# Optimization experiments

Measured on AMD Instinct MI355X. Metric: run time of the kernel, lower is better.

## Reference

```python
import jax, jax.numpy as jnp
import numpy as np

B, T, D, H = 4, 1024, 512, 8
DK = D // H
L = 2 * T - 1  # relative-position length, Transformer-XL convention


def setup_inputs() -> dict:
    key = jax.random.key(0)
    ks = jax.random.split(key, 16)
    s = 0.02  # xavier-ish init scale
    inp = {
        "query": jax.random.normal(ks[0], (B, T, D), jnp.float32),
        "key": jax.random.normal(ks[1], (B, T, D), jnp.float32),
        "value": jax.random.normal(ks[2], (B, T, D), jnp.float32),
        "pos_embedding": jax.random.normal(ks[3], (B, L, D), jnp.float32),
        "mask": jax.random.randint(ks[4], (B, T), 0, 2).astype(bool),
        # nn.Linear weights are [out, in]; y = x @ W.T + b
        "Wq": jax.random.normal(ks[5], (D, D), jnp.float32) * s,
        "bq": jnp.zeros((D,), jnp.float32),
        "Wk": jax.random.normal(ks[6], (D, D), jnp.float32) * s,
        "bk": jnp.zeros((D,), jnp.float32),
        "Wv": jax.random.normal(ks[7], (D, D), jnp.float32) * s,
        "bv": jnp.zeros((D,), jnp.float32),
        "Wr": jax.random.normal(ks[8], (D, D), jnp.float32) * s,  # rpe_proj, no bias
        "u_bias": jax.random.normal(ks[9], (H, DK), jnp.float32) * s,
        "v_bias": jax.random.normal(ks[10], (H, DK), jnp.float32) * s,
        "Wo": jax.random.normal(ks[11], (D, D), jnp.float32) * s,
        "bo": jnp.zeros((D,), jnp.float32),
    }
    return inp


def _rel_shift(x):
    # x: [B, H, T, L] -> Transformer-XL pad/reshape/slice shift, keep first L//2+1 cols
    b, h, t, l = x.shape
    x = jnp.pad(x, ((0, 0), (0, 0), (0, 0), (1, 0)))        # [B,H,T,L+1]
    x = x.reshape(b, h, l + 1, t)[:, :, 1:, :]               # drop first row
    x = x.reshape(b, h, t, l)
    return x[..., : l // 2 + 1]                              # [B,H,T,T]


def reference(query, key, value, pos_embedding, mask,
              Wq, bq, Wk, bk, Wv, bv, Wr, u_bias, v_bias, Wo, bo):
    b = query.shape[0]
    q = (query @ Wq.T + bq).reshape(b, -1, H, DK)            # [B,T,H,dk]
    k = (key @ Wk.T + bk).reshape(b, -1, H, DK)              # [B,T,H,dk]
    v = (value @ Wv.T + bv).reshape(b, -1, H, DK)            # [B,T,H,dk]
    r = (pos_embedding @ Wr.T).reshape(b, -1, H, DK)         # [B,L,H,dk]

    main = jnp.einsum('bthd,bshd->bhts', q + u_bias, k)      # content score
    rpe = jnp.einsum('bthd,blhd->bhtl', q + v_bias, r)       # [B,H,T,L]

    scores = (main + _rel_shift(rpe)) / np.sqrt(DK).astype(np.float32)
    scores = jnp.where(mask[:, None, None, :],
                       jnp.asarray(1e-4, scores.dtype), scores)
    attn = jax.nn.softmax(scores, axis=-1)                   # dropout off (eval)

    out = jnp.einsum('bhts,bshd->bhtd', attn, v)             # [B,H,T,dk]
    # Faithful to original: view(B,-1,d_model) WITHOUT transposing heads back
    out = out.reshape(b, -1, D)                              # [B,T,D] (head-interleaved)
    return out @ Wo.T + bo
```

## Files before the change

### kernel.cpp

```cpp
#include <hip/hip_runtime.h>
#include <stdint.h>
#include <stddef.h>

#define B_ 4
#define T_ 1024
#define D_ 512
#define H_ 8
#define DK_ 64
#define L_ 2047
#define LP_ 2048

typedef __attribute__((ext_vector_type(8))) short short8;
typedef __attribute__((ext_vector_type(4))) short short4_t;
typedef __attribute__((ext_vector_type(4))) float f32x4;
typedef __attribute__((ext_vector_type(8))) __bf16 bf16x8;

static __device__ __forceinline__ short f2bf(float f) {
  union { float f; unsigned u; } x; x.f = f;
  unsigned r = x.u + 0x7fffu + ((x.u >> 16) & 1u);
  return (short)(r >> 16);
}

static __device__ __forceinline__ f32x4 mfma16(bf16x8 a, bf16x8 b, f32x4 c) {
  return __builtin_amdgcn_mfma_f32_16x16x32_bf16(a, b, c, 0, 0, 0);
}

static __device__ __forceinline__ bf16x8 ldbf8(const short* p) {
  return *(const bf16x8*)p;
}

__global__ __launch_bounds__(256) void convert_kernel(
    const float* __restrict__ qin, const float* __restrict__ kin, const float* __restrict__ vin,
    const float* __restrict__ pin,
    const float* __restrict__ Wq, const float* __restrict__ Wk, const float* __restrict__ Wv,
    const float* __restrict__ Wr, const float* __restrict__ Wo,
    const unsigned char* __restrict__ mraw,
    short* __restrict__ dst, float* __restrict__ mask_f)
{
  if (blockIdx.x == 11518) {
    __shared__ int fmis, fany;
    if (threadIdx.x == 0) { fmis = 0; fany = 0; }
    __syncthreads();
    int lm = 0, la = 0;
    for (int i = threadIdx.x; i < B_ * T_; i += 256) {
      unsigned char c = mraw[i];
      if (c) { la = 1; if (i & 3) lm = 1; }
    }
    if (lm) atomicOr(&fmis, 1);
    if (la) atomicOr(&fany, 1);
    __syncthreads();
    int mmode = fmis ? 0 : (fany ? 1 : 2);
    const int* mi = (const int*)mraw;
    for (int i = threadIdx.x; i < B_ * T_; i += 256) {
      int mv = (mmode == 0) ? (int)mraw[i] : (mmode == 1 ? mi[i] : 0);
      mask_f[i] = mv ? 1.0f : 0.0f;
    }
    return;
  }
  int gid = blockIdx.x * 256 + threadIdx.x;
  const float* src; int base;
  if      (gid < 524288)  { src = qin; base = 0; }
  else if (gid < 1048576) { src = kin; base = 524288; }
  else if (gid < 1572864) { src = vin; base = 1048576; }
  else if (gid < 2620928) { src = pin; base = 1572864; }
  else if (gid < 2686464) { src = Wq;  base = 2620928; }
  else if (gid < 2752000) { src = Wk;  base = 2686464; }
  else if (gid < 2817536) { src = Wv;  base = 2752000; }
  else if (gid < 2883072) { src = Wr;  base = 2817536; }
  else                    { src = Wo;  base = 2883072; }
  f32x4 val = ((const f32x4*)src)[gid - base];
  short4_t o;
  o[0] = f2bf(val[0]); o[1] = f2bf(val[1]); o[2] = f2bf(val[2]); o[3] = f2bf(val[3]);
  ((short4_t*)dst)[gid] = o;
}

__global__ __launch_bounds__(256) void proj_gemm(
    const short* __restrict__ qkv_bf, const short* __restrict__ pos_bf,
    const short* __restrict__ W_bf, const short* __restrict__ ao_bf,
    int variant,
    short* __restrict__ quO, short* __restrict__ qvO, short* __restrict__ khO,
    short* __restrict__ vtO, short* __restrict__ rhO, float* __restrict__ outF,
    const float* __restrict__ bq, const float* __restrict__ bk_,
    const float* __restrict__ bv_, const float* __restrict__ bo_,
    const float* __restrict__ ub, const float* __restrict__ vb)
{
  const int bid = blockIdx.x;
  const short* A; const short* W;
  int Mtotal, mode, m0, n0;
  if (variant == 0) {
    if (bid < 768) {
      int zz = bid >> 8, r2 = bid & 255;
      m0 = (r2 >> 3) * 128; n0 = (r2 & 7) * 64;
      A = qkv_bf + (size_t)zz * 2097152; W = W_bf + (size_t)zz * 262144;
      Mtotal = 4096; mode = zz;
    } else {
      int r2 = bid - 768;
      m0 = (r2 >> 3) * 128; n0 = (r2 & 7) * 64;
      A = pos_bf; W = W_bf + 786432;
      Mtotal = 8188; mode = 3;
    }
  } else {
    m0 = (bid >> 3) * 128; n0 = (bid & 7) * 64;
    A = ao_bf; W = W_bf + 1048576;
    Mtotal = 4096; mode = 4;
  }
  __shared__ __align__(16) short As[2][128 * 64];
  __shared__ __align__(16) short Bs[2][64 * 64];
  const int tid = threadIdx.x;
  const int lane = tid & 63, wid = tid >> 6;
  const int wr = wid >> 1, wc = wid & 1;
  const int l15 = lane & 15, l4 = lane >> 4;

  const int trow = tid >> 3;
  const int tcol = (((tid & 7) ^ (trow & 7)) << 3);
  const int wbase = wid * 512;

  auto STAGE = [&](int buf, int kt) {
#pragma unroll
    for (int j = 0; j < 4; j++) {
      int row = j * 32 + trow;
      int srow = m0 + row; if (srow > Mtotal - 1) srow = Mtotal - 1;
      __builtin_amdgcn_global_load_lds(
          (const __attribute__((address_space(1))) unsigned int*)(A + (size_t)srow * 512 + kt + tcol),
          (__attribute__((address_space(3))) unsigned int*)(&As[buf][j * 2048 + wbase]), 16, 0, 0);
    }
#pragma unroll
    for (int j = 0; j < 2; j++) {
      int row = j * 32 + trow;
      __builtin_amdgcn_global_load_lds(
          (const __attribute__((address_space(1))) unsigned int*)(W + (size_t)(n0 + row) * 512 + kt + tcol),
          (__attribute__((address_space(3))) unsigned int*)(&Bs[buf][j * 2048 + wbase]), 16, 0, 0);
    }
  };

  f32x4 acc[4][2] = {};
  STAGE(0, 0);
  __syncthreads();

  for (int it = 0; it < 8; ++it) {
    const int cur = it & 1;
    if (it < 7) STAGE(cur ^ 1, (it + 1) * 64);
    __builtin_amdgcn_s_setprio(1);
#pragma unroll
    for (int kf = 0; kf < 2; kf++) {
      const int colA = ((kf * 4 + l4) ^ (l15 & 7)) << 3;
      bf16x8 af[4], bf2[2];
#pragma unroll
      for (int rf = 0; rf < 4; rf++)
        af[rf] = ldbf8(&As[cur][(wr * 64 + rf * 16 + l15) * 64 + colA]);
#pragma unroll
      for (int cf = 0; cf < 2; cf++)
        bf2[cf] = ldbf8(&Bs[cur][(wc * 32 + cf * 16 + l15) * 64 + colA]);
#pragma unroll
      for (int rf = 0; rf < 4; rf++)
#pragma unroll
        for (int cf = 0; cf < 2; cf++)
          acc[rf][cf] = mfma16(af[rf], bf2[cf], acc[rf][cf]);
    }
    __builtin_amdgcn_s_setprio(0);
    __syncthreads();
  }

#pragma unroll
  for (int cf = 0; cf < 2; cf++) {
    int n = n0 + wc * 32 + cf * 16 + l15;
    float bias = 0.f, ubv = 0.f, vbv = 0.f;
    if (mode == 0) { bias = bq[n]; ubv = ub[n]; vbv = vb[n]; }
    else if (mode == 1) bias = bk_[n];
    else if (mode == 2) bias = bv_[n];
    else if (mode == 4) bias = bo_[n];
    int hh = n >> 6, dk = n & 63;
#pragma unroll
    for (int rf = 0; rf < 4; rf++) {
#pragma unroll
      for (int reg = 0; reg < 4; reg++) {
        int m = m0 + wr * 64 + rf * 16 + l4 * 4 + reg;
        float val = acc[rf][cf][reg] + bias;
        if (mode == 0) {
          int bb = m >> 10, t = m & 1023;
          size_t ad = ((size_t)(bb * H_ + hh) * T_ + t) * DK_ + dk;
          quO[ad] = f2bf(val + ubv);
          qvO[ad] = f2bf(val + vbv);
        } else if (mode == 1) {
          int bb = m >> 10, t = m & 1023;
          khO[((size_t)(bb * H_ + hh) * T_ + t) * DK_ + dk] = f2bf(val);
        } else if (mode == 2) {
          int bb = m >> 10, t = m & 1023;
          vtO[((size_t)(bb * H_ + hh) * DK_ + dk) * T_ + t] = f2bf(val);
        } else if (mode == 3) {
          if (m < B_ * L_) {
            int bb = m / L_;
            int ll = m - bb * L_;
            rhO[((size_t)(bb * H_ + hh) * LP_ + ll) * DK_ + dk] = f2bf(val);
          }
        } else {
          outF[(size_t)m * D_ + n] = val;
        }
      }
    }
  }
}

__global__ __launch_bounds__(256) void attn_kernel(
    const short* __restrict__ qu, const short* __restrict__ qv,
    const short* __restrict__ kh, const short* __restrict__ vt,
    const short* __restrict__ rh, const float* __restrict__ mask_f,
    short* __restrict__ attnout)
{
  const int tid = threadIdx.x;
  const int lane = tid & 63;
  const int w = tid >> 6;
  const int l15 = lane & 15, l4 = lane >> 4;
  const int bid = blockIdx.x;
  const int xcd = bid & 7, slot = bid >> 3;
  const int bh = (slot >> 4) * 8 + xcd;
  const int b = bh >> 3;
  const int t0b = (slot & 15) * 64;
  const int t0w = t0b + w * 16;
  const int woff = 48 - w * 16;

  __shared__ __align__(16) short Ks[2][64 * 64];
  __shared__ __align__(16) short Vs[2][64 * 64];
  __shared__ __align__(16) short Rs[2][128 * 64];
  __shared__ __align__(16) short Ps[4][16 * 64];

  const short* kB = kh + (size_t)bh * T_ * DK_;
  const short* vB = vt + (size_t)bh * DK_ * T_;
  const short* rB = rh + (size_t)bh * LP_ * DK_;
  const float* mB = mask_f + b * T_;

  const short* quB = qu + ((size_t)bh * T_ + t0w + l15) * DK_ + l4 * 8;
  const short* qvB = qv + ((size_t)bh * T_ + t0w + l15) * DK_ + l4 * 8;
  bf16x8 quf0 = ldbf8(quB), quf1 = ldbf8(quB + 32);
  bf16x8 qvf0 = ldbf8(qvB), qvf1 = ldbf8(qvB + 32);

  const short8 ones_s = {(short)0x3F80, (short)0x3F80, (short)0x3F80, (short)0x3F80,
                         (short)0x3F80, (short)0x3F80, (short)0x3F80, (short)0x3F80};
  const bf16x8 ones8 = __builtin_bit_cast(bf16x8, ones_s);

  const int trow = tid >> 3;
  const int tcol = (((tid & 7) ^ ((tid >> 3) & 7)) << 3);
  const int wbase = w * 512;

  auto STAGE = [&](int buf, int s0) {
    const int l0b = 960 + s0 - t0b;
#pragma unroll
    for (int j = 0; j < 2; j++) {
      __builtin_amdgcn_global_load_lds(
          (const __attribute__((address_space(1))) unsigned int*)(kB + (size_t)(s0 + trow + j * 32) * 64 + tcol),
          (__attribute__((address_space(3))) unsigned int*)(&Ks[buf][j * 2048 + wbase]), 16, 0, 0);
      __builtin_amdgcn_global_load_lds(
          (const __attribute__((address_space(1))) unsigned int*)(vB + (size_t)(trow + j * 32) * T_ + s0 + tcol),
          (__attribute__((address_space(3))) unsigned int*)(&Vs[buf][j * 2048 + wbase]), 16, 0, 0);
    }
#pragma unroll
    for (int j = 0; j < 4; j++) {
      __builtin_amdgcn_global_load_lds(
          (const __attribute__((address_space(1))) unsigned int*)(rB + (size_t)(l0b + trow + j * 32) * 64 + tcol),
          (__attribute__((address_space(3))) unsigned int*)(&Rs[buf][j * 2048 + wbase]), 16, 0, 0);
    }
  };

  f32x4 accO[4] = {};
  f32x4 sum_acc = {};

  STAGE(0, 0);
  __syncthreads();

  const int swz = (l15 & 7) << 3;

  for (int it = 0; it < 16; ++it) {
    const int s0 = it << 6;
    const int cur = it & 1;
    if (it < 15) STAGE(cur ^ 1, s0 + 64);

    float mk[4];
#pragma unroll
    for (int cf = 0; cf < 4; cf++) mk[cf] = mB[s0 + cf * 16 + l15];

    f32x4 sacc[4] = {};
    f32x4 gacc[5] = {};
    __builtin_amdgcn_s_setprio(1);
#pragma unroll
    for (int kf = 0; kf < 2; kf++) {
      const int col = (kf * 32 + l4 * 8) ^ swz;
      bf16x8 qf = kf ? quf1 : quf0;
      bf16x8 vf_ = kf ? qvf1 : qvf0;
#pragma unroll
      for (int cf = 0; cf < 4; cf++)
        sacc[cf] = mfma16(qf, ldbf8(&Ks[cur][(cf * 16 + l15) * 64 + col]), sacc[cf]);
#pragma unroll
      for (int gf = 0; gf < 5; gf++)
        gacc[gf] = mfma16(vf_, ldbf8(&Rs[cur][(woff + gf * 16 + l15) * 64 + col]), gacc[gf]);
    }
    __builtin_amdgcn_s_setprio(0);

    float p[4][4];
#pragma unroll
    for (int r = 0; r < 4; r++) {
      const int tl = l4 * 4 + r;
      const int e = l15 + 15 - tl;
      const int src = (lane & 48) | (e & 15);
      float sh0 = __shfl(gacc[0][r], src);
      float sh1 = __shfl(gacc[1][r], src);
      float sh2 = __shfl(gacc[2][r], src);
      float sh3 = __shfl(gacc[3][r], src);
      float sh4 = __shfl(gacc[4][r], src);
      float ga[4] = {sh0, sh1, sh2, sh3};
      float gb[4] = {sh1, sh2, sh3, sh4};
#pragma unroll
      for (int cf = 0; cf < 4; cf++) {
        float gg = (e < 16) ? ga[cf] : gb[cf];
        float lg = (sacc[cf][r] + gg) * 0.125f;
        lg = (mk[cf] != 0.f) ? 1e-4f : lg;
        p[r][cf] = __expf(lg);
      }
    }

#pragma unroll
    for (int r = 0; r < 4; r++) {
      const int tl = l4 * 4 + r;
      const int sw2 = (tl & 7) << 3;
#pragma unroll
      for (int cf = 0; cf < 4; cf++)
        Ps[w][tl * 64 + ((cf * 16 + l15) ^ sw2)] = f2bf(p[r][cf]);
    }

    __builtin_amdgcn_s_setprio(1);
#pragma unroll
    for (int kf = 0; kf < 2; kf++) {
      const int kc = kf * 32 + l4 * 8;
      bf16x8 pa = ldbf8(&Ps[w][l15 * 64 + (kc ^ swz)]);
      sum_acc = mfma16(pa, ones8, sum_acc);
#pragma unroll
      for (int vf = 0; vf < 4; vf++)
        accO[vf] = mfma16(pa, ldbf8(&Vs[cur][(vf * 16 + l15) * 64 + (kc ^ swz)]), accO[vf]);
    }
    __builtin_amdgcn_s_setprio(0);
    __syncthreads();
  }

#pragma unroll
  for (int r = 0; r < 4; r++) {
    const int tl = l4 * 4 + r;
    float inv = 1.0f / sum_acc[r];
#pragma unroll
    for (int vf = 0; vf < 4; vf++) {
      float val = accO[vf][r] * inv;
      attnout[((size_t)bh * T_ + t0w + tl) * DK_ + vf * 16 + l15] = f2bf(val);
    }
  }
}

extern "C" void kernel_launch(void* const* d_in, const int* in_sizes, int n_in,
                              void* d_out, int out_size, void* d_ws, size_t ws_size,
                              hipStream_t stream) {
  const float* qin = (const float*)d_in[0];
  const float* kin = (const float*)d_in[1];
  const float* vin = (const float*)d_in[2];
  const float* pin = (const float*)d_in[3];
  const unsigned char* mraw = (const unsigned char*)d_in[4];
  const float* Wq = (const float*)d_in[5];
  const float* bq = (const float*)d_in[6];
  const float* Wk = (const float*)d_in[7];
  const float* bk = (const float*)d_in[8];
  const float* Wv = (const float*)d_in[9];
  const float* bv = (const float*)d_in[10];
  const float* Wr = (const float*)d_in[11];
  const float* ub = (const float*)d_in[12];
  const float* vb = (const float*)d_in[13];
  const float* Wo = (const float*)d_in[14];
  const float* bo = (const float*)d_in[15];
  float* out = (float*)d_out;
  char* ws = (char*)d_ws;

  short* qkv_bf = (short*)(ws + 0);
  short* pos_bf = (short*)(ws + 12582912);
  short* W_bf   = (short*)(ws + 20967424);
  float* mask_f = (float*)(ws + 23588864);
  short* quW    = (short*)(ws + 23605248);
  short* qvW    = (short*)(ws + 27799552);
  short* khW    = (short*)(ws + 31993856);
  short* vtW    = (short*)(ws + 36188160);
  short* rhW    = (short*)(ws + 40382464);
  short* aoW    = (short*)(ws + 48771072);

  convert_kernel<<<dim3(11519), dim3(256), 0, stream>>>(
      qin, kin, vin, pin, Wq, Wk, Wv, Wr, Wo, mraw, qkv_bf, mask_f);
  proj_gemm<<<dim3(1280), dim3(256), 0, stream>>>(
      qkv_bf, pos_bf, W_bf, aoW, 0, quW, qvW, khW, vtW, rhW, nullptr,
      bq, bk, bv, bo, ub, vb);
  attn_kernel<<<dim3(512), dim3(256), 0, stream>>>(
      quW, qvW, khW, vtW, rhW, mask_f, aoW);
  proj_gemm<<<dim3(256), dim3(256), 0, stream>>>(
      qkv_bf, pos_bf, W_bf, aoW, 1, quW, qvW, khW, vtW, rhW, out,
      bq, bk, bv, bo, ub, vb);
}
```

Baseline: 109.8 us.

## Fuse fp32-to-bf16 activation conversion into projection GEMM A-tile staging

The separate conversion pass over query/key/value/pos_embedding is removed. The projection GEMM now loads fp32 A tiles into registers, converts them with packed bf16 conversion instructions, and writes them to swizzled LDS after the MFMA loop, so the prefetch overlaps compute. This drops a large bf16 write and re-read of activations. The weight-only convert kernel stays, the GEMM is templated on variant, and block indices are remapped so consecutive blocks land on different XCD-strided tiles. The cost is doubled global A-read bytes in the GEMM (fp32 instead of bf16), plus extra register pressure and a VALU conversion step.

```diff
diff --git a/kernel.cpp b/kernel.cpp
--- a/kernel.cpp
+++ b/kernel.cpp
@@ -13,6 +13,7 @@
 typedef __attribute__((ext_vector_type(8))) short short8;
 typedef __attribute__((ext_vector_type(4))) short short4_t;
 typedef __attribute__((ext_vector_type(4))) float f32x4;
+typedef __attribute__((ext_vector_type(4))) unsigned int u32x4;
 typedef __attribute__((ext_vector_type(8))) __bf16 bf16x8;
 
 static __device__ __forceinline__ short f2bf(float f) {
@@ -21,6 +22,12 @@
   return (short)(r >> 16);
 }
 
+static __device__ __forceinline__ unsigned cvtpk(float lo, float hi) {
+  unsigned r;
+  asm("v_cvt_pk_bf16_f32 %0, %1, %2" : "=v"(r) : "v"(lo), "v"(hi));
+  return r;
+}
+
 static __device__ __forceinline__ f32x4 mfma16(bf16x8 a, bf16x8 b, f32x4 c) {
   return __builtin_amdgcn_mfma_f32_16x16x32_bf16(a, b, c, 0, 0, 0);
 }
@@ -29,15 +36,13 @@
   return *(const bf16x8*)p;
 }
 
-__global__ __launch_bounds__(256) void convert_kernel(
-    const float* __restrict__ qin, const float* __restrict__ kin, const float* __restrict__ vin,
-    const float* __restrict__ pin,
+__global__ __launch_bounds__(256) void convertW_kernel(
     const float* __restrict__ Wq, const float* __restrict__ Wk, const float* __restrict__ Wv,
     const float* __restrict__ Wr, const float* __restrict__ Wo,
     const unsigned char* __restrict__ mraw,
-    short* __restrict__ dst, float* __restrict__ mask_f)
+    short* __restrict__ W_bf, float* __restrict__ mask_f)
 {
-  if (blockIdx.x == 11518) {
+  if (blockIdx.x == 1280) {
     __shared__ int fmis, fany;
     if (threadIdx.x == 0) { fmis = 0; fany = 0; }
     __syncthreads();
@@ -59,49 +64,50 @@
   }
   int gid = blockIdx.x * 256 + threadIdx.x;
   const float* src; int base;
-  if      (gid < 524288)  { src = qin; base = 0; }
-  else if (gid < 1048576) { src = kin; base = 524288; }
-  else if (gid < 1572864) { src = vin; base = 1048576; }
-  else if (gid < 2620928) { src = pin; base = 1572864; }
-  else if (gid < 2686464) { src = Wq;  base = 2620928; }
-  else if (gid < 2752000) { src = Wk;  base = 2686464; }
-  else if (gid < 2817536) { src = Wv;  base = 2752000; }
-  else if (gid < 2883072) { src = Wr;  base = 2817536; }
-  else                    { src = Wo;  base = 2883072; }
+  if      (gid <  65536) { src = Wq; base = 0; }
+  else if (gid < 131072) { src = Wk; base = 65536; }
+  else if (gid < 196608) { src = Wv; base = 131072; }
+  else if (gid < 262144) { src = Wr; base = 196608; }
+  else                   { src = Wo; base = 262144; }
   f32x4 val = ((const f32x4*)src)[gid - base];
   short4_t o;
   o[0] = f2bf(val[0]); o[1] = f2bf(val[1]); o[2] = f2bf(val[2]); o[3] = f2bf(val[3]);
-  ((short4_t*)dst)[gid] = o;
-}
-
+  ((short4_t*)W_bf)[gid] = o;
+}
+
+template<int VARIANT>
 __global__ __launch_bounds__(256) void proj_gemm(
-    const short* __restrict__ qkv_bf, const short* __restrict__ pos_bf,
+    const float* __restrict__ qin, const float* __restrict__ kin,
+    const float* __restrict__ vin, const float* __restrict__ pin,
     const short* __restrict__ W_bf, const short* __restrict__ ao_bf,
-    int variant,
     short* __restrict__ quO, short* __restrict__ qvO, short* __restrict__ khO,
     short* __restrict__ vtO, short* __restrict__ rhO, float* __restrict__ outF,
     const float* __restrict__ bq, const float* __restrict__ bk_,
     const float* __restrict__ bv_, const float* __restrict__ bo_,
     const float* __restrict__ ub, const float* __restrict__ vb)
 {
-  const int bid = blockIdx.x;
-  const short* A; const short* W;
+  const int bid0 = blockIdx.x;
+  constexpr int PER = (VARIANT == 0) ? 160 : 32;
+  const int bid = (bid0 & 7) * PER + (bid0 >> 3);
+
+  const float* Afp = nullptr; const short* Abf = nullptr; const short* W;
   int Mtotal, mode, m0, n0;
-  if (variant == 0) {
+  if constexpr (VARIANT == 0) {
     if (bid < 768) {
       int zz = bid >> 8, r2 = bid & 255;
       m0 = (r2 >> 3) * 128; n0 = (r2 & 7) * 64;
-      A = qkv_bf + (size_t)zz * 2097152; W = W_bf + (size_t)zz * 262144;
+      Afp = (zz == 0) ? qin : (zz == 1) ? kin : vin;
+      W = W_bf + (size_t)zz * 262144;
       Mtotal = 4096; mode = zz;
     } else {
       int r2 = bid - 768;
       m0 = (r2 >> 3) * 128; n0 = (r2 & 7) * 64;
-      A = pos_bf; W = W_bf + 786432;
+      Afp = pin; W = W_bf + 786432;
       Mtotal = 8188; mode = 3;
     }
   } else {
     m0 = (bid >> 3) * 128; n0 = (bid & 7) * 64;
-    A = ao_bf; W = W_bf + 1048576;
+    Abf = ao_bf; W = W_bf + 1048576;
     Mtotal = 4096; mode = 4;
   }
   __shared__ __align__(16) short As[2][128 * 64];
@@ -110,36 +116,61 @@
   const int lane = tid & 63, wid = tid >> 6;
   const int wr = wid >> 1, wc = wid & 1;
   const int l15 = lane & 15, l4 = lane >> 4;
-
   const int trow = tid >> 3;
-  const int tcol = (((tid & 7) ^ (trow & 7)) << 3);
+  const int s8 = tid & 7;
+  const int tcolsw = ((s8 ^ (trow & 7)) << 3);
   const int wbase = wid * 512;
 
-  auto STAGE = [&](int buf, int kt) {
+  f32x4 va[4][2];
+  auto LOADA = [&](int kt) {
 #pragma unroll
     for (int j = 0; j < 4; j++) {
-      int row = j * 32 + trow;
-      int srow = m0 + row; if (srow > Mtotal - 1) srow = Mtotal - 1;
+      int srow = m0 + j * 32 + trow; if (srow > Mtotal - 1) srow = Mtotal - 1;
+      const f32x4* p = (const f32x4*)(Afp + (size_t)srow * 512 + kt + s8 * 8);
+      va[j][0] = p[0]; va[j][1] = p[1];
+    }
+  };
+  auto WRITEA = [&](int buf) {
+#pragma unroll
+    for (int j = 0; j < 4; j++) {
+      u32x4 wv;
+      wv[0] = cvtpk(va[j][0][0], va[j][0][1]);
+      wv[1] = cvtpk(va[j][0][2], va[j][0][3]);
+      wv[2] = cvtpk(va[j][1][0], va[j][1][1]);
+      wv[3] = cvtpk(va[j][1][2], va[j][1][3]);
+      *(u32x4*)&As[buf][(j * 32 + trow) * 64 + tcolsw] = wv;
+    }
+  };
+  auto STAGEA1 = [&](int buf, int kt) {
+#pragma unroll
+    for (int j = 0; j < 4; j++) {
+      int srow = m0 + j * 32 + trow; if (srow > 4095) srow = 4095;
       __builtin_amdgcn_global_load_lds(
-          (const __attribute__((address_space(1))) unsigned int*)(A + (size_t)srow * 512 + kt + tcol),
+          (const __attribute__((address_space(1))) unsigned int*)(Abf + (size_t)srow * 512 + kt + tcolsw),
           (__attribute__((address_space(3))) unsigned int*)(&As[buf][j * 2048 + wbase]), 16, 0, 0);
     }
+  };
+  auto STAGEW = [&](int buf, int kt) {
 #pragma unroll
     for (int j = 0; j < 2; j++) {
       int row = j * 32 + trow;
       __builtin_amdgcn_global_load_lds(
-          (const __attribute__((address_space(1))) unsigned int*)(W + (size_t)(n0 + row) * 512 + kt + tcol),
+          (const __attribute__((address_space(1))) unsigned int*)(W + (size_t)(n0 + row) * 512 + kt + tcolsw),
           (__attribute__((address_space(3))) unsigned int*)(&Bs[buf][j * 2048 + wbase]), 16, 0, 0);
     }
   };
 
   f32x4 acc[4][2] = {};
-  STAGE(0, 0);
+  if constexpr (VARIANT == 0) { LOADA(0); STAGEW(0, 0); WRITEA(0); }
+  else                        { STAGEA1(0, 0); STAGEW(0, 0); }
   __syncthreads();
 
   for (int it = 0; it < 8; ++it) {
     const int cur = it & 1;
-    if (it < 7) STAGE(cur ^ 1, (it + 1) * 64);
+    if (it < 7) {
+      if constexpr (VARIANT == 0) { LOADA((it + 1) * 64); STAGEW(cur ^ 1, (it + 1) * 64); }
+      else                        { STAGEA1(cur ^ 1, (it + 1) * 64); STAGEW(cur ^ 1, (it + 1) * 64); }
+    }
     __builtin_amdgcn_s_setprio(1);
 #pragma unroll
     for (int kf = 0; kf < 2; kf++) {
@@ -158,6 +189,7 @@
           acc[rf][cf] = mfma16(af[rf], bf2[cf], acc[rf][cf]);
     }
     __builtin_amdgcn_s_setprio(0);
+    if constexpr (VARIANT == 0) { if (it < 7) WRITEA(cur ^ 1); }
     __syncthreads();
   }
 
@@ -374,8 +406,6 @@
   float* out = (float*)d_out;
   char* ws = (char*)d_ws;
 
-  short* qkv_bf = (short*)(ws + 0);
-  short* pos_bf = (short*)(ws + 12582912);
   short* W_bf   = (short*)(ws + 20967424);
   float* mask_f = (float*)(ws + 23588864);
   short* quW    = (short*)(ws + 23605248);
@@ -385,14 +415,14 @@
   short* rhW    = (short*)(ws + 40382464);
   short* aoW    = (short*)(ws + 48771072);
 
-  convert_kernel<<<dim3(11519), dim3(256), 0, stream>>>(
-      qin, kin, vin, pin, Wq, Wk, Wv, Wr, Wo, mraw, qkv_bf, mask_f);
-  proj_gemm<<<dim3(1280), dim3(256), 0, stream>>>(
-      qkv_bf, pos_bf, W_bf, aoW, 0, quW, qvW, khW, vtW, rhW, nullptr,
+  convertW_kernel<<<dim3(1281), dim3(256), 0, stream>>>(
+      Wq, Wk, Wv, Wr, Wo, mraw, W_bf, mask_f);
+  proj_gemm<0><<<dim3(1280), dim3(256), 0, stream>>>(
+      qin, kin, vin, pin, W_bf, aoW, quW, qvW, khW, vtW, rhW, nullptr,
       bq, bk, bv, bo, ub, vb);
   attn_kernel<<<dim3(512), dim3(256), 0, stream>>>(
       quW, qvW, khW, vtW, rhW, mask_f, aoW);
-  proj_gemm<<<dim3(256), dim3(256), 0, stream>>>(
-      qkv_bf, pos_bf, W_bf, aoW, 1, quW, qvW, khW, vtW, rhW, out,
+  proj_gemm<1><<<dim3(256), dim3(256), 0, stream>>>(
+      qin, kin, vin, pin, W_bf, aoW, quW, qvW, khW, vtW, rhW, out,
       bq, bk, bv, bo, ub, vb);
 }
```

Result: faster. 97.12 us (-11.5%).

## Triple-buffer projection GEMM with vmcnt waits and XCD-aware block remap

Applied to the files above, without the earlier changes.

The projection GEMM moves from a two-stage to a three-stage LDS ring. Each iteration waits on a partial vmcnt count and one barrier, replacing the full __syncthreads after every step, so two tiles stay in flight during compute. Block IDs are remapped so that blocks with consecutive blockIdx values, which go to different XCDs, work on tiles that are far apart, and each XCD gets a contiguous run of tiles that share A and W data in its L2. The variant argument becomes a template parameter, and the extra buffer raises LDS per block from 48KB to 72KB, which may lower occupancy.

```diff
diff --git a/kernel.cpp b/kernel.cpp
--- a/kernel.cpp
+++ b/kernel.cpp
@@ -13,6 +13,7 @@
 typedef __attribute__((ext_vector_type(8))) short short8;
 typedef __attribute__((ext_vector_type(4))) short short4_t;
 typedef __attribute__((ext_vector_type(4))) float f32x4;
+typedef __attribute__((ext_vector_type(4))) unsigned int u32x4;
 typedef __attribute__((ext_vector_type(8))) __bf16 bf16x8;
 
 static __device__ __forceinline__ short f2bf(float f) {
@@ -74,20 +75,23 @@
   ((short4_t*)dst)[gid] = o;
 }
 
+template<int VARIANT>
 __global__ __launch_bounds__(256) void proj_gemm(
     const short* __restrict__ qkv_bf, const short* __restrict__ pos_bf,
     const short* __restrict__ W_bf, const short* __restrict__ ao_bf,
-    int variant,
     short* __restrict__ quO, short* __restrict__ qvO, short* __restrict__ khO,
     short* __restrict__ vtO, short* __restrict__ rhO, float* __restrict__ outF,
     const float* __restrict__ bq, const float* __restrict__ bk_,
     const float* __restrict__ bv_, const float* __restrict__ bo_,
     const float* __restrict__ ub, const float* __restrict__ vb)
 {
-  const int bid = blockIdx.x;
+  const int bid0 = blockIdx.x;
+  constexpr int PER = (VARIANT == 0) ? 160 : 32;
+  const int bid = (bid0 & 7) * PER + (bid0 >> 3);
+
   const short* A; const short* W;
   int Mtotal, mode, m0, n0;
-  if (variant == 0) {
+  if constexpr (VARIANT == 0) {
     if (bid < 768) {
       int zz = bid >> 8, r2 = bid & 255;
       m0 = (r2 >> 3) * 128; n0 = (r2 & 7) * 64;
@@ -104,42 +108,44 @@
     A = ao_bf; W = W_bf + 1048576;
     Mtotal = 4096; mode = 4;
   }
-  __shared__ __align__(16) short As[2][128 * 64];
-  __shared__ __align__(16) short Bs[2][64 * 64];
+  __shared__ __align__(16) short As[3][128 * 64];
+  __shared__ __align__(16) short Bs[3][64 * 64];
   const int tid = threadIdx.x;
   const int lane = tid & 63, wid = tid >> 6;
   const int wr = wid >> 1, wc = wid & 1;
   const int l15 = lane & 15, l4 = lane >> 4;
-
   const int trow = tid >> 3;
-  const int tcol = (((tid & 7) ^ (trow & 7)) << 3);
+  const int tcolsw = (((tid & 7) ^ (trow & 7)) << 3);
   const int wbase = wid * 512;
 
   auto STAGE = [&](int buf, int kt) {
 #pragma unroll
     for (int j = 0; j < 4; j++) {
-      int row = j * 32 + trow;
-      int srow = m0 + row; if (srow > Mtotal - 1) srow = Mtotal - 1;
+      int srow = m0 + j * 32 + trow; if (srow > Mtotal - 1) srow = Mtotal - 1;
       __builtin_amdgcn_global_load_lds(
-          (const __attribute__((address_space(1))) unsigned int*)(A + (size_t)srow * 512 + kt + tcol),
+          (const __attribute__((address_space(1))) unsigned int*)(A + (size_t)srow * 512 + kt + tcolsw),
           (__attribute__((address_space(3))) unsigned int*)(&As[buf][j * 2048 + wbase]), 16, 0, 0);
     }
 #pragma unroll
     for (int j = 0; j < 2; j++) {
       int row = j * 32 + trow;
       __builtin_amdgcn_global_load_lds(
-          (const __attribute__((address_space(1))) unsigned int*)(W + (size_t)(n0 + row) * 512 + kt + tcol),
+          (const __attribute__((address_space(1))) unsigned int*)(W + (size_t)(n0 + row) * 512 + kt + tcolsw),
           (__attribute__((address_space(3))) unsigned int*)(&Bs[buf][j * 2048 + wbase]), 16, 0, 0);
     }
   };
 
   f32x4 acc[4][2] = {};
   STAGE(0, 0);
-  __syncthreads();
-
+  STAGE(1, 64);
+
+#pragma unroll
   for (int it = 0; it < 8; ++it) {
-    const int cur = it & 1;
-    if (it < 7) STAGE(cur ^ 1, (it + 1) * 64);
+    if (it < 7) asm volatile("s_waitcnt vmcnt(6)" ::: "memory");
+    else        asm volatile("s_waitcnt vmcnt(0)" ::: "memory");
+    __builtin_amdgcn_s_barrier();
+    if (it < 6) STAGE((it + 2) % 3, (it + 2) * 64);
+    const int cur = it % 3;
     __builtin_amdgcn_s_setprio(1);
 #pragma unroll
     for (int kf = 0; kf < 2; kf++) {
@@ -158,7 +164,6 @@
           acc[rf][cf] = mfma16(af[rf], bf2[cf], acc[rf][cf]);
     }
     __builtin_amdgcn_s_setprio(0);
-    __syncthreads();
   }
 
 #pragma unroll
@@ -387,12 +392,12 @@
 
   convert_kernel<<<dim3(11519), dim3(256), 0, stream>>>(
       qin, kin, vin, pin, Wq, Wk, Wv, Wr, Wo, mraw, qkv_bf, mask_f);
-  proj_gemm<<<dim3(1280), dim3(256), 0, stream>>>(
-      qkv_bf, pos_bf, W_bf, aoW, 0, quW, qvW, khW, vtW, rhW, nullptr,
+  proj_gemm<0><<<dim3(1280), dim3(256), 0, stream>>>(
+      qkv_bf, pos_bf, W_bf, aoW, quW, qvW, khW, vtW, rhW, nullptr,
       bq, bk, bv, bo, ub, vb);
   attn_kernel<<<dim3(512), dim3(256), 0, stream>>>(
       quW, qvW, khW, vtW, rhW, mask_f, aoW);
-  proj_gemm<<<dim3(256), dim3(256), 0, stream>>>(
-      qkv_bf, pos_bf, W_bf, aoW, 1, quW, qvW, khW, vtW, rhW, out,
+  proj_gemm<1><<<dim3(256), dim3(256), 0, stream>>>(
+      qkv_bf, pos_bf, W_bf, aoW, quW, qvW, khW, vtW, rhW, out,
       bq, bk, bv, bo, ub, vb);
 }
```

New measurement: 102.5 us. -6.7%, faster.
